# Performance work log

Hardware: AMD Instinct MI355X
Metric: run time of the kernel (lower is better)

Reference implementation:

```python
import jax, jax.numpy as jnp
import numpy as np

B, D, L = 16, 256, 200
T = 1000   # max_frame_length
K = 3      # kernel_size
DW, DC = 4, 2


def setup_inputs() -> dict:
    key = jax.random.key(0)
    ks = jax.random.split(key, 16)
    plen = jax.random.randint(ks[0], (B,), 150, L + 1)
    pm = jnp.arange(L)[None, :] < plen[:, None]              # (B,L) True=valid
    phoneme_mask = pm[:, None, :]                            # (B,1,L)
    durations = jax.random.uniform(ks[1], (B, L), minval=1.0, maxval=8.0) * pm
    phoneme = jax.random.normal(ks[2], (B, D, L), dtype=jnp.float32)
    s = 0.05
    params = {
        'Wpw': jax.random.normal(ks[3], (D, D)) * s, 'bpw': jnp.zeros((D,)),
        'Cw': jax.random.normal(ks[4], (8, D, K)) * s, 'cbw': jnp.zeros((8,)),
        'Mw': jax.random.normal(ks[5], (10, DW)) * s, 'mbw': jnp.zeros((DW,)),
        'Lw': jax.random.normal(ks[6], (DW * D, D)) * s, 'lbw': jnp.zeros((D,)),
        'Wpc': jax.random.normal(ks[7], (D, D)) * s, 'bpc': jnp.zeros((D,)),
        'Cc': jax.random.normal(ks[8], (8, D, K)) * s, 'cbc': jnp.zeros((8,)),
        'Mc': jax.random.normal(ks[9], (10, DC)) * s, 'mbc': jnp.zeros((DC,)),
        'Lc': jax.random.normal(ks[10], (DW * DC, D)) * s, 'lbc': jnp.zeros((D,)),
        'Wo': jax.random.normal(ks[11], (D, 2 * D)) * s, 'bo': jnp.zeros((2 * D,)),
    }
    return {'durations': durations, 'phoneme': phoneme, 'phoneme_mask': phoneme_mask, **params}


def _conv_swish(x, W1, b1, Ck, cb, pm):
    # 1x1 conv (proj) then kernel-K 'same' conv then SiLU; mask padded phones
    h = jnp.einsum('od,bdl->bol', W1, x) + b1[None, :, None]
    h = jax.lax.conv_general_dilated(h, Ck, (1,), 'SAME',
                                     dimension_numbers=('NCH', 'OIH', 'NCH')) + cb[None, :, None]
    h = jax.nn.silu(h)
    h = jnp.where(pm[:, None, :], h, 0.0)
    return h.transpose(0, 2, 1)  # (B, L, 8)


def _mlp(S, E, h, M, mb):
    # concat start/end boundary scalars with per-phone conv features -> (B,T,L,10)
    feat = jnp.concatenate([S[..., None], E[..., None],
                            jnp.broadcast_to(h[:, None], (B, T, L, 8))], axis=-1)
    return jax.nn.silu(feat @ M + mb)


def _forward(durations, phoneme, phoneme_mask, Wpw, bpw, Cw, cbw, Mw, mbw, Lw, lbw,
             Wpc, bpc, Cc, cbc, Mc, mbc, Lc, lbc, Wo, bo):
    pm = phoneme_mask[:, 0, :]                                          # (B,L)
    frame_lengths = jnp.clip(jnp.round(durations.sum(-1)).astype(jnp.int32), 0, T)
    frame_mask = jnp.arange(T)[None, :] < frame_lengths[:, None]        # (B,T)
    attn_mask = frame_mask[:, :, None] & pm[:, None, :]                 # (B,T,L)
    sd = jnp.cumsum(durations, axis=-1)                                 # (B,L)
    sk = sd - durations
    t = jnp.arange(1, T + 1, dtype=durations.dtype)
    S = jnp.where(attn_mask, t[None, :, None] - sk[:, None, :], 0.0)    # (B,T,L)
    E = jnp.where(attn_mask, (sd - sk)[:, None, :], 0.0)                # (B,T,L)

    h_w = _conv_swish(phoneme, Wpw, bpw, Cw, cbw, pm)
    w = _mlp(S, E, h_w, Mw, mbw)                                        # (B,T,L,DW)
    w = jnp.where(pm[:, None, :, None], w, -jnp.inf)
    w = jax.nn.softmax(w, axis=2)                                       # softmax over phones
    w = jnp.where(frame_mask[:, :, None, None], w, 0.0)

    h_c = _conv_swish(phoneme, Wpc, bpc, Cc, cbc, pm)
    c = _mlp(S, E, h_c, Mc, mbc)                                        # (B,T,L,DC)

    wh = jnp.einsum('btlq,bdl->btqd', w, phoneme).reshape(B, T, DW * D) @ Lw + lbw
    wc = jnp.einsum('btlq,btlp->btqp', w, c).reshape(B, T, DW * DC) @ Lc + lbc
    whc = jnp.where(frame_mask[..., None], wh + wc, 0.0)                # (B,T,D)
    out = (whc @ Wo + bo).transpose(0, 2, 1)                            # (B,2D,T)
    return out, frame_mask, frame_lengths, w.transpose(0, 3, 1, 2)


def reference(durations, phoneme, phoneme_mask, Wpw, bpw, Cw, cbw, Mw, mbw, Lw, lbw,
              Wpc, bpc, Cc, cbc, Mc, mbc, Lc, lbc, Wo, bo):
    out, frame_mask, frame_lengths, w = _forward(
        durations, phoneme, phoneme_mask, Wpw, bpw, Cw, cbw, Mw, mbw, Lw, lbw,
        Wpc, bpc, Cc, cbc, Mc, mbc, Lc, lbc, Wo, bo)
    mean, log_std = jnp.split(out, 2, axis=1)                           # (B,D,T) each
    return (mean, log_std, frame_mask, frame_lengths, w)
```

## Files before the change

### kernel.cpp

```cpp
#include <hip/hip_runtime.h>
#include <hip/hip_bf16.h>
#include <math.h>

#define NB 16
#define ND 256
#define NL 200
#define NT 1000

typedef unsigned short ushort_t;
typedef __bf16 bf16x8 __attribute__((ext_vector_type(8)));
typedef float f32x4 __attribute__((ext_vector_type(4)));

#define OFF_PHT   0u
#define OFF_SK    4966400u
#define OFF_EW    4969600u
#define OFF_EC    4975744u
#define OFF_BW2   4981888u
#define OFF_BC2   4981912u
#define OFF_FL    4981936u
#define OFF_GT    11535552u
#define OFF_WOT   15221952u
#define OFF_BASE  15287488u
#define OFF_PHTB  15320256u
#define OFF_LWT   15844544u

__device__ __forceinline__ float silu_f(float x){ return x / (1.f + __expf(-x)); }
__device__ __forceinline__ ushort_t f2bf(float x){
  __hip_bfloat16 h = __float2bfloat16(x);
  return *(ushort_t*)&h;
}

__global__ __launch_bounds__(256) void k_stage1(
    const float* __restrict__ dur, const float* __restrict__ ph,
    const float* __restrict__ Wp_w, const float* __restrict__ C_w, const float* __restrict__ bp_w,
    const float* __restrict__ Wp_c, const float* __restrict__ C_c, const float* __restrict__ bp_c,
    const float* __restrict__ Wo, const float* __restrict__ Lw,
    float* __restrict__ sk_ws, int* __restrict__ fl_ws,
    float* __restrict__ o_fm, float* __restrict__ o_fl,
    float* __restrict__ Ew, float* __restrict__ Ec,
    float* __restrict__ bw2, float* __restrict__ bc2,
    ushort_t* __restrict__ WoT, ushort_t* __restrict__ LwT,
    float* __restrict__ phT, ushort_t* __restrict__ phTb)
{
  int bid = blockIdx.x, tid = threadIdx.x;
  if (bid < 16){
    int b = bid;
    __shared__ float sdur[NL];
    __shared__ float ssk[NL];
    __shared__ int sfl;
    if (tid < NL) sdur[tid] = dur[b*NL + tid];
    __syncthreads();
    if (tid == 0){
      float run = 0.f;
      for (int l = 0; l < NL; ++l){ ssk[l] = run; run += sdur[l]; }
      int fl = (int)rintf(run);
      fl = fl < 0 ? 0 : (fl > NT ? NT : fl);
      sfl = fl; fl_ws[b] = fl; o_fl[b] = (float)fl;
    }
    __syncthreads();
    if (tid < NL) sk_ws[b*NL + tid] = ssk[tid];
    for (int t = tid; t < NT; t += 256) o_fm[b*NT + t] = (t < sfl) ? 1.f : 0.f;
  } else if (bid < 1600){
    int sbid = bid - 16;
    if (sbid < 48){
      int gid = sbid*256 + tid;
      int branch = gid / 6144;
      int r = gid % 6144;
      int d = r & 255;
      int ock = r >> 8;
      int oc = ock / 3, k = ock % 3;
      const float* Wp = branch ? Wp_c : Wp_w;
      const float* C  = branch ? C_c  : C_w;
      float acc = 0.f;
      for (int i = 0; i < ND; ++i) acc += C[(oc*ND + i)*3 + k] * Wp[i*ND + d];
      (branch ? Ec : Ew)[r] = acc;
      if (d == 0){
        const float* bp = branch ? bp_c : bp_w;
        float bb = 0.f;
        for (int i = 0; i < ND; ++i) bb += C[(oc*ND + i)*3 + k] * bp[i];
        (branch ? bc2 : bw2)[ock] = bb;
      }
    } else {
      int gid = (sbid - 48)*256 + tid;
      if (gid < 131072){
        int n = gid >> 8, k = gid & 255;
        WoT[gid] = f2bf(Wo[(size_t)k*512 + n]);
      } else {
        int r = gid - 131072;
        int d = r & 255;
        int qn = r >> 8;
        int q = qn >> 8, n = qn & 255;
        LwT[r] = f2bf(Lw[((size_t)q*256 + d)*256 + n]);
      }
    }
  } else {
    int r = bid - 1600;
    int xb = r & 7, yb = (r >> 3) & 7, b = r >> 6;
    int l0 = xb*32, d0 = yb*32;
    int tx = tid & 31, ty = tid >> 5;
    __shared__ float tile[32][33];
    #pragma unroll
    for (int i = 0; i < 4; ++i){
      int d = d0 + ty + i*8, l = l0 + tx;
      tile[ty + i*8][tx] = (l < NL) ? ph[((size_t)b*ND + d)*NL + l] : 0.f;
    }
    __syncthreads();
    #pragma unroll
    for (int i = 0; i < 4; ++i){
      int l = l0 + ty + i*8, d = d0 + tx;
      float v = tile[tx][ty + i*8];
      if (l < NL) phT[((size_t)b*NL + l)*ND + d] = v;
      phTb[((size_t)b*256 + l)*ND + d] = f2bf(v);
    }
  }
}

__global__ __launch_bounds__(256) void k_stage2(
    const float* __restrict__ phT,
    const float* __restrict__ dur, const float* __restrict__ sk_ws,
    const float* __restrict__ Ew, const float* __restrict__ Ec,
    const float* __restrict__ bw2, const float* __restrict__ bc2,
    const float* __restrict__ cbw, const float* __restrict__ cbc,
    const float* __restrict__ Mw, const float* __restrict__ mbw,
    const float* __restrict__ Mc, const float* __restrict__ mbc,
    float4* __restrict__ base,
    const ushort_t* __restrict__ LwT, const ushort_t* __restrict__ phTb,
    ushort_t* __restrict__ Gt)
{
  __shared__ __align__(16) unsigned char smem[128*136*2];
  int bid = blockIdx.x, tid = threadIdx.x;
  if (bid < 256){
    int b = bid >> 4, x = bid & 15;
    if (x >= 13){
      int l0 = 208 + (x - 13)*16;
      if (tid < 32)
        base[((size_t)(b*256 + l0 + (tid >> 1)))*2 + (tid & 1)] = make_float4(0,0,0,0);
      return;
    }
    float (*sh)[17] = (float (*)[17])smem;
    int lu = tid >> 4, u = tid & 15;
    int l = x*16 + lu;
    float h = 0.f;
    if (l < NL){
      int branch = u >> 3, oc = u & 7;
      const float* E  = branch ? Ec  : Ew;
      const float* b2 = branch ? bc2 : bw2;
      float val = (branch ? cbc : cbw)[oc];
      #pragma unroll
      for (int k = 0; k < 3; ++k){
        int ll = l + k - 1;
        if (ll < 0 || ll >= NL) continue;
        float acc = b2[oc*3 + k];
        const float4* Er = (const float4*)(E + (oc*3 + k)*ND);
        const float4* pr = (const float4*)(phT + ((size_t)b*NL + ll)*ND);
        #pragma unroll 8
        for (int d = 0; d < 64; ++d){
          float4 e = Er[d], p = pr[d];
          acc += e.x*p.x + e.y*p.y + e.z*p.z + e.w*p.w;
        }
        val += acc;
      }
      float pm = (dur[b*NL + l] > 0.5f) ? 1.f : 0.f;
      h = silu_f(val) * pm;
    }
    sh[lu][u] = h;
    __syncthreads();
    if (tid < 16){
      int ll = x*16 + tid;
      float4 o0 = make_float4(0,0,0,0);
      float4 o1 = make_float4(0,0,0,0);
      if (ll < NL){
        float dl  = dur[b*NL + ll];
        float pm  = (dl > 0.5f) ? 1.f : 0.f;
        float skl = sk_ws[b*NL + ll];
        float c1[4], c2[2];
        #pragma unroll
        for (int q = 0; q < 4; ++q) c1[q] = mbw[q] + dl*Mw[4 + q] - skl*Mw[q];
        #pragma unroll
        for (int p = 0; p < 2; ++p) c2[p] = mbc[p] + dl*Mc[2 + p] - skl*Mc[p];
        #pragma unroll
        for (int j = 0; j < 8; ++j){
          float hwv = sh[tid][j], hcv = sh[tid][8 + j];
          #pragma unroll
          for (int q = 0; q < 4; ++q) c1[q] += hwv*Mw[(2 + j)*4 + q];
          #pragma unroll
          for (int p = 0; p < 2; ++p) c2[p] += hcv*Mc[(2 + j)*2 + p];
        }
        o0 = make_float4(c1[0], c1[1], c1[2], c1[3]);
        o1 = make_float4(c2[0], c2[1], pm, 0.f);
      }
      base[((size_t)(b*256 + ll))*2 + 0] = o0;
      base[((size_t)(b*256 + ll))*2 + 1] = o1;
    }
  } else {
    int r = bid - 256;
    int xb = r & 1, yb = (r >> 1) & 1, bq = r >> 2;
    int b = bq >> 2, q = bq & 3;
    int m0 = yb * 128;
    int n0 = xb * 128;
    int lane = tid & 63, wave = tid >> 6;
    int wm = wave >> 1, wn = wave & 1;
    int col = lane & 15, kg4 = lane >> 4;
    f32x4 acc[4][4] = {};
    for (int kt = 0; kt < 8; ++kt){
      int k0 = kt*32;
      bf16x8 afr[4], bfr[4];
      #pragma unroll
      for (int i = 0; i < 4; ++i)
        afr[i] = *(const bf16x8*)(LwT + ((size_t)(q*256 + m0 + wm*64 + i*16 + col))*256 + k0 + kg4*8);
      #pragma unroll
      for (int j = 0; j < 4; ++j)
        bfr[j] = *(const bf16x8*)(phTb + ((size_t)(b*256 + n0 + wn*64 + j*16 + col))*256 + k0 + kg4*8);
      #pragma unroll
      for (int i = 0; i < 4; ++i)
        #pragma unroll
        for (int j = 0; j < 4; ++j)
          acc[i][j] = __builtin_amdgcn_mfma_f32_16x16x32_bf16(afr[i], bfr[j], acc[i][j], 0, 0, 0);
    }
    ushort_t (*st2)[136] = (ushort_t (*)[136])smem;
    int rq = lane >> 4;
    #pragma unroll
    for (int i = 0; i < 4; ++i){
      #pragma unroll
      for (int rr = 0; rr < 4; ++rr){
        int rl = wm*64 + i*16 + rq*4 + rr;
        #pragma unroll
        for (int j = 0; j < 4; ++j){
          int cl = wn*64 + j*16 + col;
          st2[rl][cl] = f2bf(acc[i][j][rr]);
        }
      }
    }
    __syncthreads();
    #pragma unroll
    for (int rep = 0; rep < 8; ++rep){
      int row = rep*16 + (tid >> 4);
      int ch  = tid & 15;
      int l   = n0 + ch*8;
      if (l < NL){
        int n = m0 + row;
        *(uint4*)(Gt + ((size_t)(b*ND + n))*800 + q*NL + l) = *(const uint4*)&st2[row][ch*8];
      }
    }
  }
}

#define AP 808
#define TT 64
__global__ __launch_bounds__(1024, 4) void k_wv_fused(
    const float4* __restrict__ base,
    const int* __restrict__ fl_ws,
    const float* __restrict__ Mw, const float* __restrict__ Mc,
    const ushort_t* __restrict__ Gt,
    const float* __restrict__ Lc,
    const float* __restrict__ lbc,
    const float* __restrict__ lbw,
    const ushort_t* __restrict__ WoT,
    const float* __restrict__ bo,
    float* __restrict__ wout,
    float* __restrict__ o_mean, float* __restrict__ o_lstd)
{
  __shared__ ushort_t As[TT*AP];
  __shared__ float    wcs[TT][8];
  int b = blockIdx.x;
  int m0 = blockIdx.y * TT;
  int tid = threadIdx.x, lane = tid & 63, wave = tid >> 6;
  int col = lane & 15, kg4 = lane >> 4;
  int fl = fl_ws[b];

  if (fl <= m0){
    for (int idx = tid; idx < TT*4*50; idx += 1024){
      int tl = idx / 200;
      int rqs = idx - tl*200;
      int q = rqs / 50, seg = rqs - q*50;
      int t = m0 + tl;
      if (t < NT)
        *(float4*)&wout[(((size_t)(b*4 + q))*NT + t)*NL + seg*4] = make_float4(0,0,0,0);
    }
    for (int idx = tid; idx < 512*16; idx += 1024){
      int s = idx >> 4, j = idx & 15;
      int t0 = m0 + j*4;
      if (t0 + 3 < NT){
        float v = bo[s];
        float4 v4 = make_float4(v, v, v, v);
        if (s < ND) *(float4*)&o_mean[((size_t)b*ND + s)*NT + t0] = v4;
        else        *(float4*)&o_lstd[((size_t)b*ND + (s - ND))*NT + t0] = v4;
      }
    }
    return;
  }

  int l0 = lane*4;
  bool lv = (l0 < NL);

  #pragma unroll
  for (int s = 0; s < 4; ++s){
    int tl = wave*4 + s, t = m0 + tl;
    if (t < fl) continue;
    for (int k = l0; k < 800; k += 256){
      uint2 zz2; zz2.x = 0u; zz2.y = 0u;
      *(uint2*)&As[tl*AP + k] = zz2;
    }
    if (lane < 8) wcs[tl][lane] = 0.f;
    if (t < NT && lv){
      float4 z4 = make_float4(0,0,0,0);
      #pragma unroll
      for (int q = 0; q < 4; ++q)
        *(float4*)&wout[(((size_t)(b*4 + q))*NT + t)*NL + l0] = z4;
    }
  }

  float b0a[4][4], b1x[4], b1y[4], pmv[4];
  #pragma unroll
  for (int e = 0; e < 4; ++e){
    float4 v0 = make_float4(0,0,0,0), v1 = make_float4(0,0,0,0);
    if (lv){
      v0 = base[((size_t)(b*256 + l0 + e))*2 + 0];
      v1 = base[((size_t)(b*256 + l0 + e))*2 + 1];
    }
    b0a[e][0] = v0.x; b0a[e][1] = v0.y; b0a[e][2] = v0.z; b0a[e][3] = v0.w;
    b1x[e] = v1.x; b1y[e] = v1.y; pmv[e] = v1.z;
  }
  float mwq[4] = {Mw[0], Mw[1], Mw[2], Mw[3]};
  float mcp[2] = {Mc[0], Mc[1]};

  for (int sp = 0; sp < 2; ++sp){
    int tl0 = wave*4 + sp*2;
    int t0 = m0 + tl0;
    if (t0 >= fl) break;
    bool a1 = (t0 + 1 < fl);
    float tf[2] = {(float)(t0 + 1), (float)(t0 + 2)};

    float z[2][4][4], mx[2][4];
    #pragma unroll
    for (int u = 0; u < 2; ++u)
      #pragma unroll
      for (int q = 0; q < 4; ++q) mx[u][q] = -INFINITY;
    #pragma unroll
    for (int e = 0; e < 4; ++e){
      #pragma unroll
      for (int u = 0; u < 2; ++u){
        #pragma unroll
        for (int q = 0; q < 4; ++q){
          float sv = silu_f(b0a[e][q] + tf[u]*mwq[q]);
          float zv = (pmv[e] > 0.f) ? sv : -INFINITY;
          z[u][e][q] = zv;
          mx[u][q] = fmaxf(mx[u][q], zv);
        }
      }
    }
    #pragma unroll
    for (int u = 0; u < 2; ++u)
      #pragma unroll
      for (int q = 0; q < 4; ++q){
        float v = mx[u][q];
        #pragma unroll
        for (int off = 32; off; off >>= 1) v = fmaxf(v, __shfl_xor(v, off));
        mx[u][q] = v;
      }
    float is4[2][4] = {{0,0,0,0},{0,0,0,0}};
    #pragma unroll
    for (int e = 0; e < 4; ++e){
      #pragma unroll
      for (int u = 0; u < 2; ++u){
        #pragma unroll
        for (int q = 0; q < 4; ++q){
          float ev = (pmv[e] > 0.f) ? __expf(z[u][e][q] - mx[u][q]) : 0.f;
          z[u][e][q] = ev;
          is4[u][q] += ev;
        }
      }
    }
    #pragma unroll
    for (int u = 0; u < 2; ++u)
      #pragma unroll
      for (int q = 0; q < 4; ++q){
        float v = is4[u][q];
        #pragma unroll
        for (int off = 32; off; off >>= 1) v += __shfl_xor(v, off);
        is4[u][q] = 1.f / v;
      }
    float cv[2][4][2];
    #pragma unroll
    for (int e = 0; e < 4; ++e)
      #pragma unroll
      for (int u = 0; u < 2; ++u){
        cv[u][e][0] = silu_f(b1x[e] + tf[u]*mcp[0]);
        cv[u][e][1] = silu_f(b1y[e] + tf[u]*mcp[1]);
      }
    float wc[2][8];
    #pragma unroll
    for (int u = 0; u < 2; ++u)
      #pragma unroll
      for (int x = 0; x < 8; ++x) wc[u][x] = 0.f;
    #pragma unroll
    for (int u = 0; u < 2; ++u){
      bool act = (u == 0) || a1;
      int t = t0 + u, tl = tl0 + u;
      #pragma unroll
      for (int q = 0; q < 4; ++q){
        float w0 = z[u][0][q]*is4[u][q];
        float w1 = z[u][1][q]*is4[u][q];
        float w2 = z[u][2][q]*is4[u][q];
        float w3 = z[u][3][q]*is4[u][q];
        if (act && lv){
          *(float4*)&wout[(((size_t)(b*4 + q))*NT + t)*NL + l0] =
              make_float4(w0, w1, w2, w3);
          uint2 pk;
          pk.x = (unsigned)f2bf(w0) | ((unsigned)f2bf(w1) << 16);
          pk.y = (unsigned)f2bf(w2) | ((unsigned)f2bf(w3) << 16);
          *(uint2*)&As[tl*AP + q*NL + l0] = pk;
        }
        wc[u][q*2 + 0] += w0*cv[u][0][0] + w1*cv[u][1][0] + w2*cv[u][2][0] + w3*cv[u][3][0];
        wc[u][q*2 + 1] += w0*cv[u][0][1] + w1*cv[u][1][1] + w2*cv[u][2][1] + w3*cv[u][3][1];
      }
    }
    #pragma unroll
    for (int u = 0; u < 2; ++u){
      if (u == 1 && !a1) break;
      #pragma unroll
      for (int x = 0; x < 8; ++x){
        float v = wc[u][x];
        #pragma unroll
        for (int off = 32; off; off >>= 1) v += __shfl_xor(v, off);
        wc[u][x] = v;
      }
      if (lane == 0){
        #pragma unroll
        for (int x = 0; x < 8; ++x) wcs[tl0 + u][x] = wc[u][x];
      }
    }
  }
  __syncthreads();

  f32x4 acc[4] = {};
  const ushort_t* Gb = Gt + (size_t)b*ND*800;
  for (int kt = 0; kt < 25; ++kt){
    int k0 = kt*32;
    bf16x8 afr[4], bfr;
    #pragma unroll
    for (int i = 0; i < 4; ++i)
      afr[i] = *(const bf16x8*)(&As[(i*16 + col)*AP + k0 + kg4*8]);
    bfr = *(const bf16x8*)(Gb + ((size_t)(wave*16 + col))*800 + k0 + kg4*8);
    #pragma unroll
    for (int i = 0; i < 4; ++i)
      acc[i] = __builtin_amdgcn_mfma_f32_16x16x32_bf16(afr[i], bfr, acc[i], 0, 0, 0);
  }
  __syncthreads();

  ushort_t (*stc)[264] = (ushort_t (*)[264])As;
  {
    int rq = lane >> 4;
    int n = wave*16 + col;
    float lbn = lbc[n], lbwn = lbw[n];
    float lcn[8];
    #pragma unroll
    for (int u = 0; u < 8; ++u) lcn[u] = Lc[u*ND + n];
    #pragma unroll
    for (int i = 0; i < 4; ++i){
      #pragma unroll
      for (int r = 0; r < 4; ++r){
        int tl = i*16 + rq*4 + r;
        int t = m0 + tl;
        if (t < NT){
          float f = (t < fl) ? 1.f : 0.f;
          float vcv = lbn
            + wcs[tl][0]*lcn[0] + wcs[tl][1]*lcn[1]
            + wcs[tl][2]*lcn[2] + wcs[tl][3]*lcn[3]
            + wcs[tl][4]*lcn[4] + wcs[tl][5]*lcn[5]
            + wcs[tl][6]*lcn[6] + wcs[tl][7]*lcn[7];
          stc[tl][n] = f2bf(f * (acc[i][r] + lbwn + vcv));
        }
      }
    }
  }
  __syncthreads();

  {
    f32x4 acc2[2][4] = {};
    for (int kt = 0; kt < 8; ++kt){
      int k0 = kt*32;
      bf16x8 afr[2], bfr[4];
      #pragma unroll
      for (int j = 0; j < 4; ++j)
        bfr[j] = *(const bf16x8*)(&stc[j*16 + col][k0 + kg4*8]);
      #pragma unroll
      for (int i = 0; i < 2; ++i)
        afr[i] = *(const bf16x8*)(WoT + ((size_t)(wave*32 + i*16 + col))*ND + k0 + kg4*8);
      #pragma unroll
      for (int i = 0; i < 2; ++i)
        #pragma unroll
        for (int j = 0; j < 4; ++j)
          acc2[i][j] = __builtin_amdgcn_mfma_f32_16x16x32_bf16(afr[i], bfr[j], acc2[i][j], 0, 0, 0);
    }
    int rq = lane >> 4;
    #pragma unroll
    for (int i = 0; i < 2; ++i){
      #pragma unroll
      for (int r = 0; r < 4; ++r){
        int s = wave*32 + i*16 + rq*4 + r;
        float bov = bo[s];
        #pragma unroll
        for (int j = 0; j < 4; ++j){
          int t = m0 + j*16 + col;
          if (t < NT){
            float v = acc2[i][j][r] + bov;
            if (s < ND) o_mean[((size_t)b*ND + s)*NT + t] = v;
            else        o_lstd[((size_t)b*ND + (s - ND))*NT + t] = v;
          }
        }
      }
    }
  }
}

extern "C" void kernel_launch(void* const* d_in, const int* in_sizes, int n_in,
                              void* d_out, int out_size, void* d_ws, size_t ws_size,
                              hipStream_t stream)
{
  const float* dur = (const float*)d_in[0];
  const float* ph  = (const float*)d_in[1];
  const float* Wpw = (const float*)d_in[3];
  const float* bpw = (const float*)d_in[4];
  const float* Cw  = (const float*)d_in[5];
  const float* cbw = (const float*)d_in[6];
  const float* Mw  = (const float*)d_in[7];
  const float* mbw = (const float*)d_in[8];
  const float* Lw  = (const float*)d_in[9];
  const float* lbw = (const float*)d_in[10];
  const float* Wpc = (const float*)d_in[11];
  const float* bpc = (const float*)d_in[12];
  const float* Cc  = (const float*)d_in[13];
  const float* cbc = (const float*)d_in[14];
  const float* Mc  = (const float*)d_in[15];
  const float* mbc = (const float*)d_in[16];
  const float* Lc  = (const float*)d_in[17];
  const float* lbc = (const float*)d_in[18];
  const float* Wo  = (const float*)d_in[19];
  const float* bo  = (const float*)d_in[20];

  float* out    = (float*)d_out;
  float* o_mean = out;
  float* o_lstd = out + (size_t)NB*ND*NT;
  float* o_fm   = o_lstd + (size_t)NB*ND*NT;
  float* o_fl   = o_fm + NB*NT;
  float* o_w    = o_fl + NB;

  float* ws   = (float*)d_ws;
  float* phT  = ws + OFF_PHT;
  float* sk   = ws + OFF_SK;
  float* Ew   = ws + OFF_EW;
  float* Ec   = ws + OFF_EC;
  float* bw2  = ws + OFF_BW2;
  float* bc2  = ws + OFF_BC2;
  int*   fl   = (int*)(ws + OFF_FL);
  ushort_t* Gt   = (ushort_t*)(ws + OFF_GT);
  ushort_t* WoT  = (ushort_t*)(ws + OFF_WOT);
  float4*   base = (float4*)(ws + OFF_BASE);
  ushort_t* phTb = (ushort_t*)(ws + OFF_PHTB);
  ushort_t* LwT  = (ushort_t*)(ws + OFF_LWT);

  k_stage1<<<2624, 256, 0, stream>>>(dur, ph, Wpw, Cw, bpw, Wpc, Cc, bpc, Wo, Lw,
                                     sk, fl, o_fm, o_fl, Ew, Ec, bw2, bc2,
                                     WoT, LwT, phT, phTb);
  k_stage2<<<512, 256, 0, stream>>>(phT, dur, sk, Ew, Ec, bw2, bc2, cbw, cbc,
                                    Mw, mbw, Mc, mbc, base, LwT, phTb, Gt);
  {
    dim3 g(NB, 16);
    k_wv_fused<<<g, 1024, 0, stream>>>(base, fl, Mw, Mc, Gt, Lc, lbc, lbw,
                                       WoT, bo, o_w, o_mean, o_lstd);
  }
}
```

Measured before the change: 236.8 us.

## Merge stage1 and stage2 into a single kernel with on-the-fly transposes

Merges the two preprocessing kernels into one launch. The conv path now applies the 1x1 projection to a shared-memory window of phonemes before the K=3 conv, instead of precomputing fused conv-projection weights. The Lw·phoneme GEMM now loads and converts fp32 Lw and phoneme tiles to bf16 in shared memory, instead of reading pre-transposed bf16 workspace copies. This removes a kernel launch and several workspace round-trips, but adds strided uncoalesced global loads and redundant projection work per block.

```diff
diff --git a/kernel.cpp b/kernel.cpp
--- a/kernel.cpp
+++ b/kernel.cpp
@@ -11,18 +11,10 @@
 typedef __bf16 bf16x8 __attribute__((ext_vector_type(8)));
 typedef float f32x4 __attribute__((ext_vector_type(4)));
 
-#define OFF_PHT   0u
-#define OFF_SK    4966400u
-#define OFF_EW    4969600u
-#define OFF_EC    4975744u
-#define OFF_BW2   4981888u
-#define OFF_BC2   4981912u
 #define OFF_FL    4981936u
 #define OFF_GT    11535552u
 #define OFF_WOT   15221952u
 #define OFF_BASE  15287488u
-#define OFF_PHTB  15320256u
-#define OFF_LWT   15844544u
 
 __device__ __forceinline__ float silu_f(float x){ return x / (1.f + __expf(-x)); }
 __device__ __forceinline__ ushort_t f2bf(float x){
@@ -30,149 +22,109 @@
   return *(ushort_t*)&h;
 }
 
-__global__ __launch_bounds__(256) void k_stage1(
+__global__ __launch_bounds__(256, 2) void k_A(
     const float* __restrict__ dur, const float* __restrict__ ph,
     const float* __restrict__ Wp_w, const float* __restrict__ C_w, const float* __restrict__ bp_w,
     const float* __restrict__ Wp_c, const float* __restrict__ C_c, const float* __restrict__ bp_c,
     const float* __restrict__ Wo, const float* __restrict__ Lw,
-    float* __restrict__ sk_ws, int* __restrict__ fl_ws,
-    float* __restrict__ o_fm, float* __restrict__ o_fl,
-    float* __restrict__ Ew, float* __restrict__ Ec,
-    float* __restrict__ bw2, float* __restrict__ bc2,
-    ushort_t* __restrict__ WoT, ushort_t* __restrict__ LwT,
-    float* __restrict__ phT, ushort_t* __restrict__ phTb)
-{
-  int bid = blockIdx.x, tid = threadIdx.x;
-  if (bid < 16){
-    int b = bid;
-    __shared__ float sdur[NL];
-    __shared__ float ssk[NL];
-    __shared__ int sfl;
-    if (tid < NL) sdur[tid] = dur[b*NL + tid];
-    __syncthreads();
-    if (tid == 0){
-      float run = 0.f;
-      for (int l = 0; l < NL; ++l){ ssk[l] = run; run += sdur[l]; }
-      int fl = (int)rintf(run);
-      fl = fl < 0 ? 0 : (fl > NT ? NT : fl);
-      sfl = fl; fl_ws[b] = fl; o_fl[b] = (float)fl;
-    }
-    __syncthreads();
-    if (tid < NL) sk_ws[b*NL + tid] = ssk[tid];
-    for (int t = tid; t < NT; t += 256) o_fm[b*NT + t] = (t < sfl) ? 1.f : 0.f;
-  } else if (bid < 1600){
-    int sbid = bid - 16;
-    if (sbid < 48){
-      int gid = sbid*256 + tid;
-      int branch = gid / 6144;
-      int r = gid % 6144;
-      int d = r & 255;
-      int ock = r >> 8;
-      int oc = ock / 3, k = ock % 3;
-      const float* Wp = branch ? Wp_c : Wp_w;
-      const float* C  = branch ? C_c  : C_w;
-      float acc = 0.f;
-      for (int i = 0; i < ND; ++i) acc += C[(oc*ND + i)*3 + k] * Wp[i*ND + d];
-      (branch ? Ec : Ew)[r] = acc;
-      if (d == 0){
-        const float* bp = branch ? bp_c : bp_w;
-        float bb = 0.f;
-        for (int i = 0; i < ND; ++i) bb += C[(oc*ND + i)*3 + k] * bp[i];
-        (branch ? bc2 : bw2)[ock] = bb;
-      }
-    } else {
-      int gid = (sbid - 48)*256 + tid;
-      if (gid < 131072){
-        int n = gid >> 8, k = gid & 255;
-        WoT[gid] = f2bf(Wo[(size_t)k*512 + n]);
-      } else {
-        int r = gid - 131072;
-        int d = r & 255;
-        int qn = r >> 8;
-        int q = qn >> 8, n = qn & 255;
-        LwT[r] = f2bf(Lw[((size_t)q*256 + d)*256 + n]);
-      }
-    }
-  } else {
-    int r = bid - 1600;
-    int xb = r & 7, yb = (r >> 3) & 7, b = r >> 6;
-    int l0 = xb*32, d0 = yb*32;
-    int tx = tid & 31, ty = tid >> 5;
-    __shared__ float tile[32][33];
-    #pragma unroll
-    for (int i = 0; i < 4; ++i){
-      int d = d0 + ty + i*8, l = l0 + tx;
-      tile[ty + i*8][tx] = (l < NL) ? ph[((size_t)b*ND + d)*NL + l] : 0.f;
-    }
-    __syncthreads();
-    #pragma unroll
-    for (int i = 0; i < 4; ++i){
-      int l = l0 + ty + i*8, d = d0 + tx;
-      float v = tile[tx][ty + i*8];
-      if (l < NL) phT[((size_t)b*NL + l)*ND + d] = v;
-      phTb[((size_t)b*256 + l)*ND + d] = f2bf(v);
-    }
-  }
-}
-
-__global__ __launch_bounds__(256) void k_stage2(
-    const float* __restrict__ phT,
-    const float* __restrict__ dur, const float* __restrict__ sk_ws,
-    const float* __restrict__ Ew, const float* __restrict__ Ec,
-    const float* __restrict__ bw2, const float* __restrict__ bc2,
     const float* __restrict__ cbw, const float* __restrict__ cbc,
     const float* __restrict__ Mw, const float* __restrict__ mbw,
     const float* __restrict__ Mc, const float* __restrict__ mbc,
-    float4* __restrict__ base,
-    const ushort_t* __restrict__ LwT, const ushort_t* __restrict__ phTb,
+    int* __restrict__ fl_ws, float* __restrict__ o_fm, float* __restrict__ o_fl,
+    ushort_t* __restrict__ WoT, float4* __restrict__ base,
     ushort_t* __restrict__ Gt)
 {
-  __shared__ __align__(16) unsigned char smem[128*136*2];
+  __shared__ __align__(16) unsigned char smem[69632];
   int bid = blockIdx.x, tid = threadIdx.x;
+
   if (bid < 256){
-    int b = bid >> 4, x = bid & 15;
+    int r = bid;
+    int b = r >> 4, x = r & 15;
     if (x >= 13){
       int l0 = 208 + (x - 13)*16;
       if (tid < 32)
         base[((size_t)(b*256 + l0 + (tid >> 1)))*2 + (tid & 1)] = make_float4(0,0,0,0);
       return;
     }
-    float (*sh)[17] = (float (*)[17])smem;
-    int lu = tid >> 4, u = tid & 15;
-    int l = x*16 + lu;
-    float h = 0.f;
-    if (l < NL){
-      int branch = u >> 3, oc = u & 7;
-      const float* E  = branch ? Ec  : Ew;
-      const float* b2 = branch ? bc2 : bw2;
-      float val = (branch ? cbc : cbw)[oc];
-      #pragma unroll
-      for (int k = 0; k < 3; ++k){
-        int ll = l + k - 1;
-        if (ll < 0 || ll >= NL) continue;
-        float acc = b2[oc*3 + k];
-        const float4* Er = (const float4*)(E + (oc*3 + k)*ND);
-        const float4* pr = (const float4*)(phT + ((size_t)b*NL + ll)*ND);
-        #pragma unroll 8
-        for (int d = 0; d < 64; ++d){
-          float4 e = Er[d], p = pr[d];
-          acc += e.x*p.x + e.y*p.y + e.z*p.z + e.w*p.w;
-        }
-        val += acc;
-      }
-      float pm = (dur[b*NL + l] > 0.5f) ? 1.f : 0.f;
-      h = silu_f(val) * pm;
-    }
-    sh[lu][u] = h;
+    float* sdur = (float*)smem;
+    float* ssk  = sdur + 256;
+    float (*phs)[256] = (float (*)[256])(ssk + 256);
+    float (*Uw)[20] = (float (*)[20])((float*)phs + 18*256);
+    float (*Uc)[20] = Uw + 256;
+    float (*sh)[17] = (float (*)[17])(Uc + 256*1);
+    sh = (float (*)[17])((float*)Uc + 256*20);
+    int l0 = x*16;
+
+    if (tid < NL) sdur[tid] = dur[b*NL + tid];
+    __syncthreads();
+    if (tid == 0){
+      float run = 0.f;
+      for (int l = 0; l < NL; ++l){ ssk[l] = run; run += sdur[l]; }
+    }
+    {
+      int d = tid;
+      const float* pr = ph + ((size_t)b*ND + d)*NL;
+      #pragma unroll
+      for (int j = 0; j < 18; ++j){
+        int l = l0 - 1 + j;
+        phs[j][d] = (l >= 0 && l < NL) ? pr[l] : 0.f;
+      }
+    }
+    __syncthreads();
+    {
+      int i = tid;
+      float uw[18], uc[18];
+      float bw = bp_w[i], bc = bp_c[i];
+      #pragma unroll
+      for (int j = 0; j < 18; ++j){ uw[j] = bw; uc[j] = bc; }
+      const float4* wr = (const float4*)(Wp_w + (size_t)i*ND);
+      const float4* cr = (const float4*)(Wp_c + (size_t)i*ND);
+      for (int d4 = 0; d4 < 64; ++d4){
+        float4 a = wr[d4], c = cr[d4];
+        #pragma unroll
+        for (int j = 0; j < 18; ++j){
+          float4 p = *(const float4*)&phs[j][d4*4];
+          uw[j] += a.x*p.x + a.y*p.y + a.z*p.z + a.w*p.w;
+          uc[j] += c.x*p.x + c.y*p.y + c.z*p.z + c.w*p.w;
+        }
+      }
+      #pragma unroll
+      for (int j = 0; j < 18; ++j){
+        int l = l0 - 1 + j;
+        bool pad = (l < 0 || l >= NL);
+        Uw[i][j] = pad ? 0.f : uw[j];
+        Uc[i][j] = pad ? 0.f : uc[j];
+      }
+    }
+    __syncthreads();
+    {
+      int lu = tid >> 4, u = tid & 15;
+      int l = l0 + lu;
+      float h = 0.f;
+      if (l < NL){
+        int branch = u >> 3, oc = u & 7;
+        float (*U)[20] = branch ? Uc : Uw;
+        const float* C = branch ? C_c : C_w;
+        float val = (branch ? cbc : cbw)[oc];
+        #pragma unroll 4
+        for (int i = 0; i < ND; ++i){
+          const float* cc = C + ((size_t)oc*ND + i)*3;
+          val += cc[0]*U[i][lu] + cc[1]*U[i][lu + 1] + cc[2]*U[i][lu + 2];
+        }
+        float pm = (sdur[l] > 0.5f) ? 1.f : 0.f;
+        h = silu_f(val) * pm;
+      }
+      sh[lu][u] = h;
+    }
     __syncthreads();
     if (tid < 16){
       int ll = x*16 + tid;
       float4 o0 = make_float4(0,0,0,0);
       float4 o1 = make_float4(0,0,0,0);
       if (ll < NL){
-        float dl  = dur[b*NL + ll];
+        float dl  = sdur[ll];
         float pm  = (dl > 0.5f) ? 1.f : 0.f;
-        float skl = sk_ws[b*NL + ll];
+        float skl = ssk[ll];
         float c1[4], c2[2];
         #pragma unroll
         for (int q = 0; q < 4; ++q) c1[q] = mbw[q] + dl*Mw[4 + q] - skl*Mw[q];
@@ -192,7 +144,7 @@
       base[((size_t)(b*256 + ll))*2 + 0] = o0;
       base[((size_t)(b*256 + ll))*2 + 1] = o1;
     }
-  } else {
+  } else if (bid < 512){
     int r = bid - 256;
     int xb = r & 1, yb = (r >> 1) & 1, bq = r >> 2;
     int b = bq >> 2, q = bq & 3;
@@ -201,23 +153,61 @@
     int lane = tid & 63, wave = tid >> 6;
     int wm = wave >> 1, wn = wave & 1;
     int col = lane & 15, kg4 = lane >> 4;
+    ushort_t (*Asub)[136] = (ushort_t (*)[136])smem;
+    ushort_t (*Bsub)[136] = (ushort_t (*)[136])(smem + 34816);
+
     f32x4 acc[4][4] = {};
-    for (int kt = 0; kt < 8; ++kt){
-      int k0 = kt*32;
-      bf16x8 afr[4], bfr[4];
-      #pragma unroll
-      for (int i = 0; i < 4; ++i)
-        afr[i] = *(const bf16x8*)(LwT + ((size_t)(q*256 + m0 + wm*64 + i*16 + col))*256 + k0 + kg4*8);
-      #pragma unroll
-      for (int j = 0; j < 4; ++j)
-        bfr[j] = *(const bf16x8*)(phTb + ((size_t)(b*256 + n0 + wn*64 + j*16 + col))*256 + k0 + kg4*8);
-      #pragma unroll
-      for (int i = 0; i < 4; ++i)
+    for (int kh = 0; kh < 2; ++kh){
+      int d0 = kh*128;
+      if (tid < 128){
+        int n = m0 + tid;
+        const float* src = Lw + ((size_t)(q*256 + d0))*ND + n;
+        #pragma unroll
+        for (int dc = 0; dc < 16; ++dc){
+          ushort_t tmp[8];
+          #pragma unroll
+          for (int j = 0; j < 8; ++j)
+            tmp[j] = f2bf(src[(size_t)(dc*8 + j)*ND]);
+          *(uint4*)&Asub[tid][dc*8] = *(const uint4*)tmp;
+        }
+      } else {
+        int t2 = tid - 128;
+        int l = n0 + t2;
+        if (l < NL){
+          const float* src = ph + ((size_t)b*ND + d0)*NL + l;
+          #pragma unroll
+          for (int dc = 0; dc < 16; ++dc){
+            ushort_t tmp[8];
+            #pragma unroll
+            for (int j = 0; j < 8; ++j)
+              tmp[j] = f2bf(src[(size_t)(dc*8 + j)*NL]);
+            *(uint4*)&Bsub[t2][dc*8] = *(const uint4*)tmp;
+          }
+        } else {
+          uint4 z; z.x = z.y = z.z = z.w = 0u;
+          #pragma unroll
+          for (int dc = 0; dc < 16; ++dc) *(uint4*)&Bsub[t2][dc*8] = z;
+        }
+      }
+      __syncthreads();
+      for (int kt = 0; kt < 4; ++kt){
+        int k0 = kt*32;
+        bf16x8 afr[4], bfr[4];
+        #pragma unroll
+        for (int i = 0; i < 4; ++i)
+          afr[i] = *(const bf16x8*)&Asub[wm*64 + i*16 + col][k0 + kg4*8];
         #pragma unroll
         for (int j = 0; j < 4; ++j)
-          acc[i][j] = __builtin_amdgcn_mfma_f32_16x16x32_bf16(afr[i], bfr[j], acc[i][j], 0, 0, 0);
-    }
-    ushort_t (*st2)[136] = (ushort_t (*)[136])smem;
+          bfr[j] = *(const bf16x8*)&Bsub[wn*64 + j*16 + col][k0 + kg4*8];
+        #pragma unroll
+        for (int i = 0; i < 4; ++i)
+          #pragma unroll
+          for (int j = 0; j < 4; ++j)
+            acc[i][j] = __builtin_amdgcn_mfma_f32_16x16x32_bf16(afr[i], bfr[j], acc[i][j], 0, 0, 0);
+      }
+      __syncthreads();
+    }
+    ushort_t (*st2)[136] = Asub;
     int rq = lane >> 4;
     #pragma unroll
     for (int i = 0; i < 4; ++i){
@@ -241,6 +231,30 @@
         int n = m0 + row;
         *(uint4*)(Gt + ((size_t)(b*ND + n))*800 + q*NL + l) = *(const uint4*)&st2[row][ch*8];
       }
+    }
+  } else if (bid < 528){
+    int b = bid - 512;
+    float* sdur = (float*)smem;
+    int* sfl = (int*)(sdur + 256);
+    if (tid < NL) sdur[tid] = dur[b*NL + tid];
+    __syncthreads();
+    if (tid == 0){
+      float run = 0.f;
+      for (int l = 0; l < NL; ++l) run += sdur[l];
+      int fl = (int)rintf(run);
+      fl = fl < 0 ? 0 : (fl > NT ? NT : fl);
+      sfl[0] = fl; fl_ws[b] = fl; o_fl[b] = (float)fl;
+    }
+    __syncthreads();
+    int flv = sfl[0];
+    for (int t = tid; t < NT; t += 256) o_fm[b*NT + t] = (t < flv) ? 1.f : 0.f;
+  } else {
+    int base_id = (bid - 528)*256 + tid;
+    #pragma unroll
+    for (int rep = 0; rep < 4; ++rep){
+      int gid = rep*32768 + base_id;
+      int n = gid >> 8, k = gid & 255;
+      WoT[gid] = f2bf(Wo[(size_t)k*512 + n]);
     }
   }
 }
@@ -547,24 +561,14 @@
   float* o_w    = o_fl + NB;
 
   float* ws   = (float*)d_ws;
-  float* phT  = ws + OFF_PHT;
-  float* sk   = ws + OFF_SK;
-  float* Ew   = ws + OFF_EW;
-  float* Ec   = ws + OFF_EC;
-  float* bw2  = ws + OFF_BW2;
-  float* bc2  = ws + OFF_BC2;
   int*   fl   = (int*)(ws + OFF_FL);
   ushort_t* Gt   = (ushort_t*)(ws + OFF_GT);
   ushort_t* WoT  = (ushort_t*)(ws + OFF_WOT);
   float4*   base = (float4*)(ws + OFF_BASE);
-  ushort_t* phTb = (ushort_t*)(ws + OFF_PHTB);
-  ushort_t* LwT  = (ushort_t*)(ws + OFF_LWT);
-
-  k_stage1<<<2624, 256, 0, stream>>>(dur, ph, Wpw, Cw, bpw, Wpc, Cc, bpc, Wo, Lw,
-                                     sk, fl, o_fm, o_fl, Ew, Ec, bw2, bc2,
-                                     WoT, LwT, phT, phTb);
-  k_stage2<<<512, 256, 0, stream>>>(phT, dur, sk, Ew, Ec, bw2, bc2, cbw, cbc,
-                                    Mw, mbw, Mc, mbc, base, LwT, phTb, Gt);
+
+  k_A<<<656, 256, 0, stream>>>(dur, ph, Wpw, Cw, bpw, Wpc, Cc, bpc, Wo, Lw,
+                               cbw, cbc, Mw, mbw, Mc, mbc,
+                               fl, o_fm, o_fl, WoT, base, Gt);
   {
     dim3 g(NB, 16);
     k_wv_fused<<<g, 1024, 0, stream>>>(base, fl, Mw, Mc, Gt, Lc, lbc, lbw,
```

After: 237.9 us. No clear change (+0.5%).
